# Performance work log

Hardware: AMD Instinct MI355X
Metric: run time of the kernel (lower is better)

Reference implementation:

```python
import jax, jax.numpy as jnp
import numpy as np

THRESHOLD = 0.9
EPS = 1e-12


def setup_inputs() -> dict:
    key = jax.random.key(0)
    ks = jax.random.split(key, 7)
    B, D_in, H1, H2, D_out = 8192, 256, 512, 256, 64
    # torch Linear default init ~ U(-1/sqrt(fan_in), 1/sqrt(fan_in)); randn scaled is fine as a stand-in
    def lin(k, out_f, in_f):
        return jax.random.normal(k, (out_f, in_f), dtype=jnp.float32) / np.sqrt(in_f)
    return {
        "x": jax.random.normal(ks[0], (B, D_in), dtype=jnp.float32),
        "W1": lin(ks[1], H1, D_in),
        "b1": jax.random.normal(ks[2], (H1,), dtype=jnp.float32) * 0.01,
        "W2": lin(ks[3], H2, H1),
        "b2": jax.random.normal(ks[4], (H2,), dtype=jnp.float32) * 0.01,
        "W3": lin(ks[5], D_out, H2),
        "b3": jax.random.normal(ks[6], (D_out,), dtype=jnp.float32) * 0.01,
    }


def reference(x, W1, b1, W2, b2, W3, b3):
    # MLP: Linear -> Tanh -> Linear -> Tanh -> Linear (no tanh on last)
    h1 = jnp.tanh(x @ W1.T + b1)          # [B, 512]
    h2 = jnp.tanh(h1 @ W2.T + b2)         # [B, 256]
    out = h2 @ W3.T + b3                  # [B, 64]

    # Pairwise state fidelity: (normalized dot)^2, thresholded adjacency (diag excluded)
    norms = jnp.linalg.norm(out, axis=-1, keepdims=True)  # [B, 1]
    normed = out / (norms + EPS)
    fid = (normed @ normed.T) ** 2                         # [B, B]
    adj = (fid >= THRESHOLD).astype(out.dtype)
    B = out.shape[0]
    adj = adj * (1.0 - jnp.eye(B, dtype=out.dtype))        # no self-edges (i < j pairs only)

    return adj @ out                                       # [B, 64]
```

## Files before the change

kernel.cpp:

```cpp
#include <hip/hip_runtime.h>
#include <hip/hip_bf16.h>
#include <math.h>

#define B_ROWS 8192
#define D_IN   256
#define H1_DIM 512
#define H2_DIM 256
#define D_OUT  64
#define EPSF   1e-12f
#define THRESH 0.9f
#define BAND_LO 0.89f
#define BAND_HI 0.91f

typedef __attribute__((ext_vector_type(8))) short short8;
typedef __attribute__((ext_vector_type(4))) float f32x4;

__device__ inline float tanh_fast(float xx) {
  const float ax = fabsf(xx);
  const float t = __expf(-2.0f * ax);
  const float r = (1.0f - t) / (1.0f + t);
  return xx < 0.0f ? -r : r;
}

__device__ inline void splitf8(float4 a, float4 b, short8& h, short8& m) {
  float v[8] = {a.x, a.y, a.z, a.w, b.x, b.y, b.z, b.w};
  short h8[8], m8[8];
#pragma unroll
  for (int e = 0; e < 8; ++e) {
    __hip_bfloat16 hb = __float2bfloat16(v[e]);
    float hf = __bfloat162float(hb);
    __hip_bfloat16 mb = __float2bfloat16(v[e] - hf);
    h8[e] = *(short*)&hb;
    m8[e] = *(short*)&mb;
  }
  h = *(short8*)h8;
  m = *(short8*)m8;
}

__global__ __launch_bounds__(512, 2)
void fused_mlp(const float* __restrict__ x,  const float* __restrict__ W1,
               const float* __restrict__ b1, const float* __restrict__ W2,
               const float* __restrict__ b2, const float* __restrict__ W3,
               const float* __restrict__ b3, float* __restrict__ out,
               short* __restrict__ vph, short* __restrict__ vpm,
               float* __restrict__ res) {
  constexpr int WC = 260;
  __shared__ __align__(16) union {
    struct { short h[8192]; short m[8192]; } xp;
    struct { short h[8192]; short m[8192]; } h2p;
  } uAB;
  __shared__ __align__(16) short h1h[16384];
  __shared__ __align__(16) short h1m[16384];
  __shared__ __align__(16) float wbuf[32 * WC];
  __shared__ float nsum[32];
  __shared__ float invn[32];

  const int tid = threadIdx.x;
  const int wave = tid >> 6, lane = tid & 63;
  const int r0 = blockIdx.x * 32;
  const int col16 = lane & 15;
  const int k8 = (lane >> 4) << 3;
  const int rbase = (lane >> 4) * 2 * 2;

  {
    float4* rz = (float4*)(res + (size_t)r0 * D_OUT);
    rz[tid] = make_float4(0.f, 0.f, 0.f, 0.f);
  }

#pragma unroll
  for (int uu = 0; uu < 2; ++uu) {
    const int u = tid + uu * 512;
    const int lu = u & 63, g = u >> 6;
    const int q = g & 7, I = g >> 3;
    const float* p = x + (size_t)(r0 + I * 16 + (lu & 15)) * D_IN + q * 32 + ((lu >> 4) << 3);
    float4 a = *(const float4*)p, b = *(const float4*)(p + 4);
    short8 hh, mm;
    splitf8(a, b, hh, mm);
    const int off = ((I * 8 + q) * 64 + lu) * 8;
    *(short8*)(uAB.xp.h + off) = hh;
    *(short8*)(uAB.xp.m + off) = mm;
  }
  __syncthreads();

  f32x4 acc1[2][4];
#pragma unroll
  for (int it = 0; it < 2; ++it)
#pragma unroll
    for (int jj = 0; jj < 4; ++jj) acc1[it][jj] = (f32x4){0.f, 0.f, 0.f, 0.f};

#pragma unroll 4
  for (int q = 0; q < 8; ++q) {
    short8 Ah[2], Am[2];
#pragma unroll
    for (int it = 0; it < 2; ++it) {
      const int off = ((it * 8 + q) * 64 + lane) * 8;
      Ah[it] = *(const short8*)(uAB.xp.h + off);
      Am[it] = *(const short8*)(uAB.xp.m + off);
    }
    short8 Bh[4], Bm[4];
#pragma unroll
    for (int jj = 0; jj < 4; ++jj) {
      const float* wp = W1 + (size_t)((wave * 4 + jj) * 16 + col16) * D_IN + q * 32 + k8;
      splitf8(*(const float4*)wp, *(const float4*)(wp + 4), Bh[jj], Bm[jj]);
    }
#pragma unroll
    for (int it = 0; it < 2; ++it)
#pragma unroll
      for (int jj = 0; jj < 4; ++jj) {
        acc1[it][jj] = __builtin_amdgcn_mfma_f32_16x16x32_bf16(Ah[it], Bh[jj], acc1[it][jj], 0, 0, 0);
        acc1[it][jj] = __builtin_amdgcn_mfma_f32_16x16x32_bf16(Ah[it], Bm[jj], acc1[it][jj], 0, 0, 0);
        acc1[it][jj] = __builtin_amdgcn_mfma_f32_16x16x32_bf16(Am[it], Bh[jj], acc1[it][jj], 0, 0, 0);
      }
  }

  float bv1[4];
#pragma unroll
  for (int jj = 0; jj < 4; ++jj) bv1[jj] = b1[(wave * 4 + jj) * 16 + col16];

#pragma unroll
  for (int h = 0; h < 2; ++h) {
    if ((wave >> 2) == h) {
#pragma unroll
      for (int it = 0; it < 2; ++it)
#pragma unroll
        for (int jj = 0; jj < 4; ++jj)
#pragma unroll
          for (int r = 0; r < 4; ++r) {
            const int row = it * 16 + rbase + r;
            const int col = ((wave & 3) * 4 + jj) * 16 + col16;
            wbuf[row * WC + col] = tanh_fast(acc1[it][jj][r] + bv1[jj]);
          }
    }
    __syncthreads();
#pragma unroll
    for (int uu = 0; uu < 2; ++uu) {
      const int u = tid + uu * 512;
      const int lu = u & 63, g = u >> 6;
      const int ql = g & 7, it = g >> 3;
      const int row = it * 16 + (lu & 15);
      const int kl = ql * 32 + ((lu >> 4) << 3);
      const float* wp = &wbuf[row * WC + kl];
      short8 hh, mm;
      splitf8(*(const float4*)wp, *(const float4*)(wp + 4), hh, mm);
      const int off = ((it * 16 + h * 8 + ql) * 64 + lu) * 8;
      *(short8*)(h1h + off) = hh;
      *(short8*)(h1m + off) = mm;
    }
    __syncthreads();
  }

  f32x4 acc2[2][2];
#pragma unroll
  for (int it = 0; it < 2; ++it)
#pragma unroll
    for (int jj = 0; jj < 2; ++jj) acc2[it][jj] = (f32x4){0.f, 0.f, 0.f, 0.f};

#pragma unroll 4
  for (int q = 0; q < 16; ++q) {
    short8 Ah[2], Am[2];
#pragma unroll
    for (int it = 0; it < 2; ++it) {
      const int off = ((it * 16 + q) * 64 + lane) * 8;
      Ah[it] = *(const short8*)(h1h + off);
      Am[it] = *(const short8*)(h1m + off);
    }
    short8 Bh[2], Bm[2];
#pragma unroll
    for (int jj = 0; jj < 2; ++jj) {
      const float* wp = W2 + (size_t)((wave * 2 + jj) * 16 + col16) * H1_DIM + q * 32 + k8;
      splitf8(*(const float4*)wp, *(const float4*)(wp + 4), Bh[jj], Bm[jj]);
    }
#pragma unroll
    for (int it = 0; it < 2; ++it)
#pragma unroll
      for (int jj = 0; jj < 2; ++jj) {
        acc2[it][jj] = __builtin_amdgcn_mfma_f32_16x16x32_bf16(Ah[it], Bh[jj], acc2[it][jj], 0, 0, 0);
        acc2[it][jj] = __builtin_amdgcn_mfma_f32_16x16x32_bf16(Ah[it], Bm[jj], acc2[it][jj], 0, 0, 0);
        acc2[it][jj] = __builtin_amdgcn_mfma_f32_16x16x32_bf16(Am[it], Bh[jj], acc2[it][jj], 0, 0, 0);
      }
  }

  {
    float bv2[2];
#pragma unroll
    for (int jj = 0; jj < 2; ++jj) bv2[jj] = b2[(wave * 2 + jj) * 16 + col16];
#pragma unroll
    for (int it = 0; it < 2; ++it)
#pragma unroll
      for (int jj = 0; jj < 2; ++jj)
#pragma unroll
        for (int r = 0; r < 4; ++r) {
          const int row = it * 16 + rbase + r;
          const int col = (wave * 2 + jj) * 16 + col16;
          wbuf[row * WC + col] = tanh_fast(acc2[it][jj][r] + bv2[jj]);
        }
  }
  __syncthreads();
#pragma unroll
  for (int uu = 0; uu < 2; ++uu) {
    const int u = tid + uu * 512;
    const int lu = u & 63, g = u >> 6;
    const int ql = g & 7, it = g >> 3;
    const int row = it * 16 + (lu & 15);
    const int kl = ql * 32 + ((lu >> 4) << 3);
    const float* wp = &wbuf[row * WC + kl];
    short8 hh, mm;
    splitf8(*(const float4*)wp, *(const float4*)(wp + 4), hh, mm);
    const int off = ((it * 8 + ql) * 64 + lu) * 8;
    *(short8*)(uAB.h2p.h + off) = hh;
    *(short8*)(uAB.h2p.m + off) = mm;
  }
  __syncthreads();

  if (wave < 4) {
    f32x4 acc3[2];
#pragma unroll
    for (int it = 0; it < 2; ++it) acc3[it] = (f32x4){0.f, 0.f, 0.f, 0.f};
#pragma unroll
    for (int q = 0; q < 8; ++q) {
      short8 Ah[2], Am[2];
#pragma unroll
      for (int it = 0; it < 2; ++it) {
        const int off = ((it * 8 + q) * 64 + lane) * 8;
        Ah[it] = *(const short8*)(uAB.h2p.h + off);
        Am[it] = *(const short8*)(uAB.h2p.m + off);
      }
      short8 Bh, Bm;
      const float* wp = W3 + (size_t)(wave * 16 + col16) * H2_DIM + q * 32 + k8;
      splitf8(*(const float4*)wp, *(const float4*)(wp + 4), Bh, Bm);
#pragma unroll
      for (int it = 0; it < 2; ++it) {
        acc3[it] = __builtin_amdgcn_mfma_f32_16x16x32_bf16(Ah[it], Bh, acc3[it], 0, 0, 0);
        acc3[it] = __builtin_amdgcn_mfma_f32_16x16x32_bf16(Ah[it], Bm, acc3[it], 0, 0, 0);
        acc3[it] = __builtin_amdgcn_mfma_f32_16x16x32_bf16(Am[it], Bh, acc3[it], 0, 0, 0);
      }
    }
    const float bv3 = b3[wave * 16 + col16];
#pragma unroll
    for (int it = 0; it < 2; ++it)
#pragma unroll
      for (int r = 0; r < 4; ++r)
        wbuf[(it * 16 + rbase + r) * WC + wave * 16 + col16] = acc3[it][r] + bv3;
  }
  __syncthreads();

  if (tid < 256) {
    const int row = tid >> 3, c0 = (tid & 7) * 8;
    const float* wp = &wbuf[row * WC + c0];
    float4 a = *(const float4*)wp, b = *(const float4*)(wp + 4);
    float s = a.x * a.x + a.y * a.y + a.z * a.z + a.w * a.w +
              b.x * b.x + b.y * b.y + b.z * b.z + b.w * b.w;
    s += __shfl_xor(s, 1, 64);
    s += __shfl_xor(s, 2, 64);
    s += __shfl_xor(s, 4, 64);
    if ((tid & 7) == 0) nsum[row] = s;
  }
  __syncthreads();
  if (tid < 32) invn[tid] = 1.0f / (sqrtf(nsum[tid]) + EPSF);
  __syncthreads();

  {
    const int row = tid >> 4, c4 = (tid & 15) * 4;
    *(float4*)(out + (size_t)(r0 + row) * D_OUT + c4) = *(const float4*)&wbuf[row * WC + c4];
  }
  if (tid < 256) {
    const int lu = tid & 63, g = tid >> 6;
    const int ql = g & 1, it = g >> 1;
    const int row = it * 16 + (lu & 15);
    const int kl = ql * 32 + ((lu >> 4) << 3);
    const float sc = invn[row];
    const float* wp = &wbuf[row * WC + kl];
    float4 a = *(const float4*)wp, b = *(const float4*)(wp + 4);
    a.x *= sc; a.y *= sc; a.z *= sc; a.w *= sc;
    b.x *= sc; b.y *= sc; b.z *= sc; b.w *= sc;
    short8 hh, mm;
    splitf8(a, b, hh, mm);
    const size_t off = (((size_t)(blockIdx.x * 2 + it) * 2 + ql) * 64 + lu) * 8;
    *(short8*)(vph + off) = hh;
    *(short8*)(vpm + off) = mm;
  }
}

__global__ __launch_bounds__(256, 2)
void gram_accum(const short* __restrict__ vph, const short* __restrict__ vpm,
                const float* __restrict__ out, float* __restrict__ res) {
  __shared__ __align__(16) short lAh[8 * 1024];
  __shared__ __align__(16) short lAm[8 * 1024];
  const int tid = threadIdx.x;
  const int wave = tid >> 6, lane = tid & 63;

  const int t = blockIdx.x;
  int I = (int)((129.0f - sqrtf(16641.0f - 8.0f * (float)t)) * 0.5f);
  if (I < 0) I = 0;
  while (64 * (I + 1) - ((I + 1) * I) / 2 <= t) ++I;
  while (64 * I - (I * (I - 1)) / 2 > t) --I;
  const int Jc = I + (t - (64 * I - (I * (I - 1)) / 2));
  const int i0 = I * 128;
  const int j0c = Jc * 128;

  {
    const size_t base = (size_t)I * 8192;
#pragma unroll
    for (int u = 0; u < 8; ++u) {
      const int item = wave * 8 + u;
      const short* src;
      short* dst;
      if (item < 16) { src = vph + base + item * 512; dst = lAh + item * 512; }
      else           { src = vpm + base + (item - 16) * 512; dst = lAm + (item - 16) * 512; }
      __builtin_amdgcn_global_load_lds(
          (const __attribute__((address_space(1))) void*)(src + lane * 8),
          (__attribute__((address_space(3))) void*)dst, 16, 0, 0);
    }
  }
  __syncthreads();

  short8 Ah[8][2];
#pragma unroll
  for (int it = 0; it < 8; ++it)
#pragma unroll
    for (int q = 0; q < 2; ++q)
      Ah[it][q] = *(const short8*)(lAh + it * 1024 + q * 512 + lane * 8);

#pragma unroll
  for (int tt = 0; tt < 2; ++tt) {
    const int jt = wave * 2 + tt;
    const int j0 = j0c + jt * 16;
    const short* jb_h = vph + (size_t)(j0 >> 4) * 1024;
    short8 Bh0 = *(const short8*)(jb_h + lane * 8);
    short8 Bh1 = *(const short8*)(jb_h + 512 + lane * 8);

    f32x4 g[8];
#pragma unroll
    for (int it = 0; it < 8; ++it) g[it] = (f32x4){0.f, 0.f, 0.f, 0.f};
#pragma unroll
    for (int it = 0; it < 8; ++it) g[it] = __builtin_amdgcn_mfma_f32_16x16x32_bf16(Ah[it][0], Bh0, g[it], 0, 0, 0);
#pragma unroll
    for (int it = 0; it < 8; ++it) g[it] = __builtin_amdgcn_mfma_f32_16x16x32_bf16(Ah[it][1], Bh1, g[it], 0, 0, 0);

    bool band = false;
#pragma unroll
    for (int it = 0; it < 8; ++it)
#pragma unroll
      for (int r = 0; r < 4; ++r) {
        const float f = g[it][r] * g[it][r];
        band = band || (f > BAND_LO && f < BAND_HI);
      }
    if (__any(band)) {
      const short* jb_m = vpm + (size_t)(j0 >> 4) * 1024;
      short8 Bm0 = *(const short8*)(jb_m + lane * 8);
      short8 Bm1 = *(const short8*)(jb_m + 512 + lane * 8);
#pragma unroll
      for (int it = 0; it < 8; ++it) g[it] = __builtin_amdgcn_mfma_f32_16x16x32_bf16(Ah[it][0], Bm0, g[it], 0, 0, 0);
#pragma unroll
      for (int it = 0; it < 8; ++it) g[it] = __builtin_amdgcn_mfma_f32_16x16x32_bf16(Ah[it][1], Bm1, g[it], 0, 0, 0);
#pragma unroll
      for (int it = 0; it < 8; ++it) {
        short8 Am0 = *(const short8*)(lAm + it * 1024 + lane * 8);
        short8 Am1 = *(const short8*)(lAm + it * 1024 + 512 + lane * 8);
        g[it] = __builtin_amdgcn_mfma_f32_16x16x32_bf16(Am0, Bh0, g[it], 0, 0, 0);
        g[it] = __builtin_amdgcn_mfma_f32_16x16x32_bf16(Am1, Bh1, g[it], 0, 0, 0);
      }
    }

    const int j = j0 + (lane & 15);
#pragma unroll
    for (int it = 0; it < 8; ++it) {
      const float m01 = fmaxf(g[it][0] * g[it][0], g[it][1] * g[it][1]);
      const float m23 = fmaxf(g[it][2] * g[it][2], g[it][3] * g[it][3]);
      if (fmaxf(m01, m23) >= THRESH) {
        const float* __restrict__ oj = out + (size_t)j * D_OUT;
#pragma unroll
        for (int r = 0; r < 4; ++r) {
          if (g[it][r] * g[it][r] >= THRESH) {
            const int i = i0 + it * 16 + (lane >> 4) * 4 + r;
            if (i < j) {
              float* __restrict__ ri = res + (size_t)i * D_OUT;
              float* __restrict__ rj = res + (size_t)j * D_OUT;
              const float* __restrict__ oi = out + (size_t)i * D_OUT;
              for (int k = 0; k < D_OUT; ++k) {
                atomicAdd(&ri[k], oj[k]);
                atomicAdd(&rj[k], oi[k]);
              }
            }
          }
        }
      }
    }
  }
}

#define MB (1024 * 1024)

extern "C" void kernel_launch(void* const* d_in, const int* in_sizes, int n_in,
                              void* d_out, int out_size, void* d_ws, size_t ws_size,
                              hipStream_t stream) {
  const float* x  = (const float*)d_in[0];
  const float* W1 = (const float*)d_in[1];
  const float* b1 = (const float*)d_in[2];
  const float* W2 = (const float*)d_in[3];
  const float* b2 = (const float*)d_in[4];
  const float* W3 = (const float*)d_in[5];
  const float* b3 = (const float*)d_in[6];
  float* res = (float*)d_out;

  char* ws = (char*)d_ws;
  float* out = (float*)(ws);
  short* vph = (short*)(ws + 2 * MB);
  short* vpm = (short*)(ws + 3 * MB);

  fused_mlp<<<256, 512, 0, stream>>>(x, W1, b1, W2, b2, W3, b3, out, vph, vpm, res);
  gram_accum<<<dim3(2080), 256, 0, stream>>>(vph, vpm, out, res);
}
```

Before: 129.1 us.

## Prepack weights, shrink MLP row tile, ballot-based atomic scatter in gram

Adds a weight prepack kernel that splits W1/W2/W3 into bf16 hi/lo fragments once per call, so the fused MLP loads MFMA-ready fragments instead of splitting weights in every block. The MLP now handles 16 rows per block over 512 blocks with a smaller, XOR-swizzled shared buffer to raise occupancy and cut bank conflicts. The gram kernel no longer stages the low-part A tiles in LDS and reads them from global only on band hits. Its per-edge atomic loop becomes a wave ballot where each lane adds one of the 64 columns, giving coalesced atomics. The costs are an extra kernel launch and more workspace.

New measurement: 117.9 us. 1.1x faster.

```diff
diff --git a/kernel.cpp b/kernel.cpp
--- a/kernel.cpp
+++ b/kernel.cpp
@@ -37,245 +37,235 @@
   m = *(short8*)m8;
 }
 
-__global__ __launch_bounds__(512, 2)
-void fused_mlp(const float* __restrict__ x,  const float* __restrict__ W1,
-               const float* __restrict__ b1, const float* __restrict__ W2,
-               const float* __restrict__ b2, const float* __restrict__ W3,
-               const float* __restrict__ b3, float* __restrict__ out,
-               short* __restrict__ vph, short* __restrict__ vpm,
-               float* __restrict__ res) {
-  constexpr int WC = 260;
-  __shared__ __align__(16) union {
-    struct { short h[8192]; short m[8192]; } xp;
-    struct { short h[8192]; short m[8192]; } h2p;
-  } uAB;
-  __shared__ __align__(16) short h1h[16384];
-  __shared__ __align__(16) short h1m[16384];
-  __shared__ __align__(16) float wbuf[32 * WC];
-  __shared__ float nsum[32];
-  __shared__ float invn[32];
+__device__ inline void rd8_swz(const float* buf, int S, int row, int kl,
+                               float4& a, float4& b) {
+  const int xr = (row & 7) << 2;
+  a = *(const float4*)&buf[(row * S + kl) ^ xr];
+  b = *(const float4*)&buf[(row * S + kl + 4) ^ xr];
+}
+
+__device__ inline void pack8(const float* __restrict__ src, short* __restrict__ dh,
+                             short* __restrict__ dm, int t, int C, int lgq) {
+  const int lane = t & 63;
+  const int g = t >> 6;
+  const int q = g & ((1 << lgq) - 1);
+  const int I = g >> lgq;
+  const int row = I * 16 + (lane & 15);
+  const int k0 = q * 32 + ((lane >> 4) << 3);
+  const float* p = src + (size_t)row * C + k0;
+  short8 hh, mm;
+  splitf8(*(const float4*)p, *(const float4*)(p + 4), hh, mm);
+  *(short8*)(dh + (size_t)t * 8) = hh;
+  *(short8*)(dm + (size_t)t * 8) = mm;
+}
+
+__global__ __launch_bounds__(256)
+void wpack(const float* __restrict__ W1, const float* __restrict__ W2,
+           const float* __restrict__ W3,
+           short* w1h, short* w1m, short* w2h, short* w2m,
+           short* w3h, short* w3m) {
+  const int b = blockIdx.x, tid = threadIdx.x;
+  if (b < 64)        pack8(W1, w1h, w1m, b * 256 + tid, 256, 3);
+  else if (b < 128)  pack8(W2, w2h, w2m, (b - 64) * 256 + tid, 512, 4);
+  else               pack8(W3, w3h, w3m, (b - 128) * 256 + tid, 256, 3);
+}
+
+__global__ __launch_bounds__(512, 4)
+void fused_mlp16(const float* __restrict__ x,
+                 const short* __restrict__ w1h, const short* __restrict__ w1m,
+                 const float* __restrict__ b1,
+                 const short* __restrict__ w2h, const short* __restrict__ w2m,
+                 const float* __restrict__ b2,
+                 const short* __restrict__ w3h, const short* __restrict__ w3m,
+                 const float* __restrict__ b3,
+                 float* __restrict__ out, short* __restrict__ vph,
+                 short* __restrict__ vpm, float* __restrict__ res) {
+  __shared__ __align__(16) char smem[49152];
+  short* xph   = (short*)smem;
+  short* xpm   = (short*)(smem + 8192);
+  float* wbuf1 = (float*)smem;
+  float* wbuf3 = (float*)smem;
+  short* h1h   = (short*)(smem + 16384);
+  short* h1m   = (short*)(smem + 32768);
+  float* wbuf2 = (float*)(smem + 16384);
+  short* h2ph  = (short*)(smem + 32768);
+  short* h2pm  = (short*)(smem + 40960);
+  __shared__ float nsum[16];
+  __shared__ float invn[16];
 
   const int tid = threadIdx.x;
   const int wave = tid >> 6, lane = tid & 63;
-  const int r0 = blockIdx.x * 32;
+  const int r0 = blockIdx.x * 16;
   const int col16 = lane & 15;
-  const int k8 = (lane >> 4) << 3;
-  const int rbase = (lane >> 4) * 2 * 2;
-
-  {
+  const int rbase = (lane >> 4) << 2;
+
+  if (tid < 256) {
     float4* rz = (float4*)(res + (size_t)r0 * D_OUT);
     rz[tid] = make_float4(0.f, 0.f, 0.f, 0.f);
   }
 
-#pragma unroll
-  for (int uu = 0; uu < 2; ++uu) {
-    const int u = tid + uu * 512;
-    const int lu = u & 63, g = u >> 6;
-    const int q = g & 7, I = g >> 3;
-    const float* p = x + (size_t)(r0 + I * 16 + (lu & 15)) * D_IN + q * 32 + ((lu >> 4) << 3);
-    float4 a = *(const float4*)p, b = *(const float4*)(p + 4);
+  {
+    const int lu = tid & 63, q = tid >> 6;
+    const float* p = x + (size_t)(r0 + (lu & 15)) * D_IN + q * 32 + ((lu >> 4) << 3);
+    short8 hh, mm;
+    splitf8(*(const float4*)p, *(const float4*)(p + 4), hh, mm);
+    const int off = (q * 64 + lu) * 8;
+    *(short8*)(xph + off) = hh;
+    *(short8*)(xpm + off) = mm;
+  }
+  __syncthreads();
+
+  f32x4 acc1[4];
+#pragma unroll
+  for (int jj = 0; jj < 4; ++jj) acc1[jj] = (f32x4){0.f, 0.f, 0.f, 0.f};
+#pragma unroll 4
+  for (int q = 0; q < 8; ++q) {
+    const int aoff = (q * 64 + lane) * 8;
+    const short8 Ah = *(const short8*)(xph + aoff);
+    const short8 Am = *(const short8*)(xpm + aoff);
+#pragma unroll
+    for (int jj = 0; jj < 4; ++jj) {
+      const int boff = (((wave * 4 + jj) * 8 + q) * 64 + lane) * 8;
+      const short8 Bh = *(const short8*)(w1h + boff);
+      const short8 Bm = *(const short8*)(w1m + boff);
+      acc1[jj] = __builtin_amdgcn_mfma_f32_16x16x32_bf16(Ah, Bh, acc1[jj], 0, 0, 0);
+      acc1[jj] = __builtin_amdgcn_mfma_f32_16x16x32_bf16(Ah, Bm, acc1[jj], 0, 0, 0);
+      acc1[jj] = __builtin_amdgcn_mfma_f32_16x16x32_bf16(Am, Bh, acc1[jj], 0, 0, 0);
+    }
+  }
+  __syncthreads();
+
+  float bv1[4];
+#pragma unroll
+  for (int jj = 0; jj < 4; ++jj) bv1[jj] = b1[(wave * 4 + jj) * 16 + col16];
+#pragma unroll
+  for (int h = 0; h < 2; ++h) {
+    if ((wave >> 2) == h) {
+#pragma unroll
+      for (int jj = 0; jj < 4; ++jj)
+#pragma unroll
+        for (int r = 0; r < 4; ++r) {
+          const int row = rbase + r;
+          const int col = ((wave & 3) * 4 + jj) * 16 + col16;
+          wbuf1[(row * 256 + col) ^ ((row & 7) << 2)] = tanh_fast(acc1[jj][r] + bv1[jj]);
+        }
+    }
+    __syncthreads();
+    {
+      const int lu = tid & 63, ql = tid >> 6;
+      const int row = lu & 15, kl = ql * 32 + ((lu >> 4) << 3);
+      float4 a, b;
+      rd8_swz(wbuf1, 256, row, kl, a, b);
+      short8 hh, mm;
+      splitf8(a, b, hh, mm);
+      const int off = ((h * 8 + ql) * 64 + lu) * 8;
+      *(short8*)(h1h + off) = hh;
+      *(short8*)(h1m + off) = mm;
+    }
+    __syncthreads();
+  }
+
+  f32x4 acc2[2];
+#pragma unroll
+  for (int jj = 0; jj < 2; ++jj) acc2[jj] = (f32x4){0.f, 0.f, 0.f, 0.f};
+#pragma unroll 4
+  for (int q = 0; q < 16; ++q) {
+    const int aoff = (q * 64 + lane) * 8;
+    const short8 Ah = *(const short8*)(h1h + aoff);
+    const short8 Am = *(const short8*)(h1m + aoff);
+#pragma unroll
+    for (int jj = 0; jj < 2; ++jj) {
+      const int boff = (((wave * 2 + jj) * 16 + q) * 64 + lane) * 8;
+      const short8 Bh = *(const short8*)(w2h + boff);
+      const short8 Bm = *(const short8*)(w2m + boff);
+      acc2[jj] = __builtin_amdgcn_mfma_f32_16x16x32_bf16(Ah, Bh, acc2[jj], 0, 0, 0);
+      acc2[jj] = __builtin_amdgcn_mfma_f32_16x16x32_bf16(Ah, Bm, acc2[jj], 0, 0, 0);
+      acc2[jj] = __builtin_amdgcn_mfma_f32_16x16x32_bf16(Am, Bh, acc2[jj], 0, 0, 0);
+    }
+  }
+  __syncthreads();
+
+  {
+    float bv2[2];
+#pragma unroll
+    for (int jj = 0; jj < 2; ++jj) bv2[jj] = b2[(wave * 2 + jj) * 16 + col16];
+#pragma unroll
+    for (int jj = 0; jj < 2; ++jj)
+#pragma unroll
+      for (int r = 0; r < 4; ++r) {
+        const int row = rbase + r;
+        const int col = (wave * 2 + jj) * 16 + col16;
+        wbuf2[(row * 256 + col) ^ ((row & 7) << 2)] = tanh_fast(acc2[jj][r] + bv2[jj]);
+      }
+  }
+  __syncthreads();
+  {
+    const int lu = tid & 63, ql = tid >> 6;
+    const int row = lu & 15, kl = ql * 32 + ((lu >> 4) << 3);
+    float4 a, b;
+    rd8_swz(wbuf2, 256, row, kl, a, b);
     short8 hh, mm;
     splitf8(a, b, hh, mm);
-    const int off = ((I * 8 + q) * 64 + lu) * 8;
-    *(short8*)(uAB.xp.h + off) = hh;
-    *(short8*)(uAB.xp.m + off) = mm;
-  }
-  __syncthreads();
-
-  f32x4 acc1[2][4];
-#pragma unroll
-  for (int it = 0; it < 2; ++it)
-#pragma unroll
-    for (int jj = 0; jj < 4; ++jj) acc1[it][jj] = (f32x4){0.f, 0.f, 0.f, 0.f};
-
+    const int off = (ql * 64 + lu) * 8;
+    *(short8*)(h2ph + off) = hh;
+    *(short8*)(h2pm + off) = mm;
+  }
+  __syncthreads();
+
+  if (wave < 4) {
+    f32x4 acc3 = (f32x4){0.f, 0.f, 0.f, 0.f};
 #pragma unroll 4
-  for (int q = 0; q < 8; ++q) {
-    short8 Ah[2], Am[2];
-#pragma unroll
-    for (int it = 0; it < 2; ++it) {
-      const int off = ((it * 8 + q) * 64 + lane) * 8;
-      Ah[it] = *(const short8*)(uAB.xp.h + off);
-      Am[it] = *(const short8*)(uAB.xp.m + off);
-    }
-    short8 Bh[4], Bm[4];
-#pragma unroll
-    for (int jj = 0; jj < 4; ++jj) {
-      const float* wp = W1 + (size_t)((wave * 4 + jj) * 16 + col16) * D_IN + q * 32 + k8;
-      splitf8(*(const float4*)wp, *(const float4*)(wp + 4), Bh[jj], Bm[jj]);
-    }
-#pragma unroll
-    for (int it = 0; it < 2; ++it)
-#pragma unroll
-      for (int jj = 0; jj < 4; ++jj) {
-        acc1[it][jj] = __builtin_amdgcn_mfma_f32_16x16x32_bf16(Ah[it], Bh[jj], acc1[it][jj], 0, 0, 0);
-        acc1[it][jj] = __builtin_amdgcn_mfma_f32_16x16x32_bf16(Ah[it], Bm[jj], acc1[it][jj], 0, 0, 0);
-        acc1[it][jj] = __builtin_amdgcn_mfma_f32_16x16x32_bf16(Am[it], Bh[jj], acc1[it][jj], 0, 0, 0);
-      }
-  }
-
-  float bv1[4];
-#pragma unroll
-  for (int jj = 0; jj < 4; ++jj) bv1[jj] = b1[(wave * 4 + jj) * 16 + col16];
-
-#pragma unroll
-  for (int h = 0; h < 2; ++h) {
-    if ((wave >> 2) == h) {
-#pragma unroll
-      for (int it = 0; it < 2; ++it)
-#pragma unroll
-        for (int jj = 0; jj < 4; ++jj)
-#pragma unroll
-          for (int r = 0; r < 4; ++r) {
-            const int row = it * 16 + rbase + r;
-            const int col = ((wave & 3) * 4 + jj) * 16 + col16;
-            wbuf[row * WC + col] = tanh_fast(acc1[it][jj][r] + bv1[jj]);
-          }
-    }
-    __syncthreads();
-#pragma unroll
-    for (int uu = 0; uu < 2; ++uu) {
-      const int u = tid + uu * 512;
-      const int lu = u & 63, g = u >> 6;
-      const int ql = g & 7, it = g >> 3;
-      const int row = it * 16 + (lu & 15);
-      const int kl = ql * 32 + ((lu >> 4) << 3);
-      const float* wp = &wbuf[row * WC + kl];
-      short8 hh, mm;
-      splitf8(*(const float4*)wp, *(const float4*)(wp + 4), hh, mm);
-      const int off = ((it * 16 + h * 8 + ql) * 64 + lu) * 8;
-      *(short8*)(h1h + off) = hh;
-      *(short8*)(h1m + off) = mm;
-    }
-    __syncthreads();
-  }
-
-  f32x4 acc2[2][2];
-#pragma unroll
-  for (int it = 0; it < 2; ++it)
-#pragma unroll
-    for (int jj = 0; jj < 2; ++jj) acc2[it][jj] = (f32x4){0.f, 0.f, 0.f, 0.f};
-
-#pragma unroll 4
-  for (int q = 0; q < 16; ++q) {
-    short8 Ah[2], Am[2];
-#pragma unroll
-    for (int it = 0; it < 2; ++it) {
-      const int off = ((it * 16 + q) * 64 + lane) * 8;
-      Ah[it] = *(const short8*)(h1h + off);
-      Am[it] = *(const short8*)(h1m + off);
-    }
-    short8 Bh[2], Bm[2];
-#pragma unroll
-    for (int jj = 0; jj < 2; ++jj) {
-      const float* wp = W2 + (size_t)((wave * 2 + jj) * 16 + col16) * H1_DIM + q * 32 + k8;
-      splitf8(*(const float4*)wp, *(const float4*)(wp + 4), Bh[jj], Bm[jj]);
-    }
-#pragma unroll
-    for (int it = 0; it < 2; ++it)
-#pragma unroll
-      for (int jj = 0; jj < 2; ++jj) {
-        acc2[it][jj] = __builtin_amdgcn_mfma_f32_16x16x32_bf16(Ah[it], Bh[jj], acc2[it][jj], 0, 0, 0);
-        acc2[it][jj] = __builtin_amdgcn_mfma_f32_16x16x32_bf16(Ah[it], Bm[jj], acc2[it][jj], 0, 0, 0);
-        acc2[it][jj] = __builtin_amdgcn_mfma_f32_16x16x32_bf16(Am[it], Bh[jj], acc2[it][jj], 0, 0, 0);
-      }
-  }
-
-  {
-    float bv2[2];
-#pragma unroll
-    for (int jj = 0; jj < 2; ++jj) bv2[jj] = b2[(wave * 2 + jj) * 16 + col16];
-#pragma unroll
-    for (int it = 0; it < 2; ++it)
-#pragma unroll
-      for (int jj = 0; jj < 2; ++jj)
-#pragma unroll
-        for (int r = 0; r < 4; ++r) {
-          const int row = it * 16 + rbase + r;
-          const int col = (wave * 2 + jj) * 16 + col16;
-          wbuf[row * WC + col] = tanh_fast(acc2[it][jj][r] + bv2[jj]);
-        }
-  }
-  __syncthreads();
-#pragma unroll
-  for (int uu = 0; uu < 2; ++uu) {
-    const int u = tid + uu * 512;
-    const int lu = u & 63, g = u >> 6;
-    const int ql = g & 7, it = g >> 3;
-    const int row = it * 16 + (lu & 15);
-    const int kl = ql * 32 + ((lu >> 4) << 3);
-    const float* wp = &wbuf[row * WC + kl];
-    short8 hh, mm;
-    splitf8(*(const float4*)wp, *(const float4*)(wp + 4), hh, mm);
-    const int off = ((it * 8 + ql) * 64 + lu) * 8;
-    *(short8*)(uAB.h2p.h + off) = hh;
-    *(short8*)(uAB.h2p.m + off) = mm;
-  }
-  __syncthreads();
-
-  if (wave < 4) {
-    f32x4 acc3[2];
-#pragma unroll
-    for (int it = 0; it < 2; ++it) acc3[it] = (f32x4){0.f, 0.f, 0.f, 0.f};
-#pragma unroll
     for (int q = 0; q < 8; ++q) {
-      short8 Ah[2], Am[2];
-#pragma unroll
-      for (int it = 0; it < 2; ++it) {
-        const int off = ((it * 8 + q) * 64 + lane) * 8;
-        Ah[it] = *(const short8*)(uAB.h2p.h + off);
-        Am[it] = *(const short8*)(uAB.h2p.m + off);
-      }
-      short8 Bh, Bm;
-      const float* wp = W3 + (size_t)(wave * 16 + col16) * H2_DIM + q * 32 + k8;
-      splitf8(*(const float4*)wp, *(const float4*)(wp + 4), Bh, Bm);
-#pragma unroll
-      for (int it = 0; it < 2; ++it) {
-        acc3[it] = __builtin_amdgcn_mfma_f32_16x16x32_bf16(Ah[it], Bh, acc3[it], 0, 0, 0);
-        acc3[it] = __builtin_amdgcn_mfma_f32_16x16x32_bf16(Ah[it], Bm, acc3[it], 0, 0, 0);
-        acc3[it] = __builtin_amdgcn_mfma_f32_16x16x32_bf16(Am[it], Bh, acc3[it], 0, 0, 0);
-      }
+      const int aoff = (q * 64 + lane) * 8;
+      const short8 Ah = *(const short8*)(h2ph + aoff);
+      const short8 Am = *(const short8*)(h2pm + aoff);
+      const int boff = ((wave * 8 + q) * 64 + lane) * 8;
+      const short8 Bh = *(const short8*)(w3h + boff);
+      const short8 Bm = *(const short8*)(w3m + boff);
+      acc3 = __builtin_amdgcn_mfma_f32_16x16x32_bf16(Ah, Bh, acc3, 0, 0, 0);
+      acc3 = __builtin_amdgcn_mfma_f32_16x16x32_bf16(Ah, Bm, acc3, 0, 0, 0);
+      acc3 = __builtin_amdgcn_mfma_f32_16x16x32_bf16(Am, Bh, acc3, 0, 0, 0);
     }
     const float bv3 = b3[wave * 16 + col16];
 #pragma unroll
-    for (int it = 0; it < 2; ++it)
-#pragma unroll
-      for (int r = 0; r < 4; ++r)
-        wbuf[(it * 16 + rbase + r) * WC + wave * 16 + col16] = acc3[it][r] + bv3;
+    for (int r = 0; r < 4; ++r) {
+      const int row = rbase + r;
+      const int col = wave * 16 + col16;
+      wbuf3[(row * 64 + col) ^ ((row & 7) << 2)] = acc3[r] + bv3;
+    }
   }
   __syncthreads();
 
   if (tid < 256) {
-    const int row = tid >> 3, c0 = (tid & 7) * 8;
-    const float* wp = &wbuf[row * WC + c0];
-    float4 a = *(const float4*)wp, b = *(const float4*)(wp + 4);
-    float s = a.x * a.x + a.y * a.y + a.z * a.z + a.w * a.w +
-              b.x * b.x + b.y * b.y + b.z * b.z + b.w * b.w;
+    const int row = tid >> 4, c4 = (tid & 15) * 4;
+    const float4 a = *(const float4*)&wbuf3[(row * 64 + c4) ^ ((row & 7) << 2)];
+    float s = a.x * a.x + a.y * a.y + a.z * a.z + a.w * a.w;
     s += __shfl_xor(s, 1, 64);
     s += __shfl_xor(s, 2, 64);
     s += __shfl_xor(s, 4, 64);
-    if ((tid & 7) == 0) nsum[row] = s;
-  }
-  __syncthreads();
-  if (tid < 32) invn[tid] = 1.0f / (sqrtf(nsum[tid]) + EPSF);
-  __syncthreads();
-
-  {
+    s += __shfl_xor(s, 8, 64);
+    if ((tid & 15) == 0) nsum[row] = s;
+  }
+  __syncthreads();
+  if (tid < 16) invn[tid] = 1.0f / (sqrtf(nsum[tid]) + EPSF);
+  __syncthreads();
+
+  if (tid < 256) {
     const int row = tid >> 4, c4 = (tid & 15) * 4;
-    *(float4*)(out + (size_t)(r0 + row) * D_OUT + c4) = *(const float4*)&wbuf[row * WC + c4];
-  }
-  if (tid < 256) {
-    const int lu = tid & 63, g = tid >> 6;
-    const int ql = g & 1, it = g >> 1;
-    const int row = it * 16 + (lu & 15);
-    const int kl = ql * 32 + ((lu >> 4) << 3);
+    *(float4*)(out + (size_t)(r0 + row) * D_OUT + c4) =
+        *(const float4*)&wbuf3[(row * 64 + c4) ^ ((row & 7) << 2)];
+  }
+  if (tid < 128) {
+    const int lu = tid & 63, ql = tid >> 6;
+    const int row = lu & 15, kl = ql * 32 + ((lu >> 4) << 3);
     const float sc = invn[row];
-    const float* wp = &wbuf[row * WC + kl];
-    float4 a = *(const float4*)wp, b = *(const float4*)(wp + 4);
+    float4 a, b;
+    rd8_swz(wbuf3, 64, row, kl, a, b);
     a.x *= sc; a.y *= sc; a.z *= sc; a.w *= sc;
     b.x *= sc; b.y *= sc; b.z *= sc; b.w *= sc;
     short8 hh, mm;
     splitf8(a, b, hh, mm);
-    const size_t off = (((size_t)(blockIdx.x * 2 + it) * 2 + ql) * 64 + lu) * 8;
+    const size_t off = (((size_t)blockIdx.x * 2 + ql) * 64 + lu) * 8;
     *(short8*)(vph + off) = hh;
     *(short8*)(vpm + off) = mm;
   }
@@ -285,7 +275,6 @@
 void gram_accum(const short* __restrict__ vph, const short* __restrict__ vpm,
                 const float* __restrict__ out, float* __restrict__ res) {
   __shared__ __align__(16) short lAh[8 * 1024];
-  __shared__ __align__(16) short lAm[8 * 1024];
   const int tid = threadIdx.x;
   const int wave = tid >> 6, lane = tid & 63;
 
@@ -301,15 +290,11 @@
   {
     const size_t base = (size_t)I * 8192;
 #pragma unroll
-    for (int u = 0; u < 8; ++u) {
-      const int item = wave * 8 + u;
-      const short* src;
-      short* dst;
-      if (item < 16) { src = vph + base + item * 512; dst = lAh + item * 512; }
-      else           { src = vpm + base + (item - 16) * 512; dst = lAm + (item - 16) * 512; }
+    for (int u = 0; u < 4; ++u) {
+      const int item = wave * 4 + u;
       __builtin_amdgcn_global_load_lds(
-          (const __attribute__((address_space(1))) void*)(src + lane * 8),
-          (__attribute__((address_space(3))) void*)dst, 16, 0, 0);
+          (const __attribute__((address_space(1))) void*)(vph + base + item * 512 + lane * 8),
+          (__attribute__((address_space(3))) void*)(lAh + item * 512), 16, 0, 0);
     }
   }
   __syncthreads();
@@ -355,41 +340,36 @@
       for (int it = 0; it < 8; ++it) g[it] = __builtin_amdgcn_mfma_f32_16x16x32_bf16(Ah[it][1], Bm1, g[it], 0, 0, 0);
 #pragma unroll
       for (int it = 0; it < 8; ++it) {
-        short8 Am0 = *(const short8*)(lAm + it * 1024 + lane * 8);
-        short8 Am1 = *(const short8*)(lAm + it * 1024 + 512 + lane * 8);
+        const size_t abase = (size_t)((i0 >> 4) + it) * 1024;
+        short8 Am0 = *(const short8*)(vpm + abase + lane * 8);
+        short8 Am1 = *(const short8*)(vpm + abase + 512 + lane * 8);
         g[it] = __builtin_amdgcn_mfma_f32_16x16x32_bf16(Am0, Bh0, g[it], 0, 0, 0);
         g[it] = __builtin_amdgcn_mfma_f32_16x16x32_bf16(Am1, Bh1, g[it], 0, 0, 0);
       }
     }
 
-    const int j = j0 + (lane & 15);
-#pragma unroll
-    for (int it = 0; it < 8; ++it) {
-      const float m01 = fmaxf(g[it][0] * g[it][0], g[it][1] * g[it][1]);
-      const float m23 = fmaxf(g[it][2] * g[it][2], g[it][3] * g[it][3]);
-      if (fmaxf(m01, m23) >= THRESH) {
-        const float* __restrict__ oj = out + (size_t)j * D_OUT;
-#pragma unroll
-        for (int r = 0; r < 4; ++r) {
-          if (g[it][r] * g[it][r] >= THRESH) {
-            const int i = i0 + it * 16 + (lane >> 4) * 4 + r;
-            if (i < j) {
-              float* __restrict__ ri = res + (size_t)i * D_OUT;
-              float* __restrict__ rj = res + (size_t)j * D_OUT;
-              const float* __restrict__ oi = out + (size_t)i * D_OUT;
-              for (int k = 0; k < D_OUT; ++k) {
-                atomicAdd(&ri[k], oj[k]);
-                atomicAdd(&rj[k], oi[k]);
-              }
-            }
-          }
+    const int jl = j0 + (lane & 15);
+#pragma unroll
+    for (int it = 0; it < 8; ++it)
+#pragma unroll
+      for (int r = 0; r < 4; ++r) {
+        const int il = i0 + it * 16 + (lane >> 4) * 4 + r;
+        unsigned long long m =
+            __ballot((g[it][r] * g[it][r] >= THRESH) && (il < jl));
+        while (m) {
+          const int s = __builtin_ctzll(m);
+          m &= m - 1;
+          const int js = j0 + (s & 15);
+          const int is = i0 + it * 16 + ((s >> 4) << 2) + r;
+          atomicAdd(res + (size_t)is * D_OUT + lane, out[(size_t)js * D_OUT + lane]);
+          atomicAdd(res + (size_t)js * D_OUT + lane, out[(size_t)is * D_OUT + lane]);
         }
       }
-    }
   }
 }
 
 #define MB (1024 * 1024)
+#define KB 1024
 
 extern "C" void kernel_launch(void* const* d_in, const int* in_sizes, int n_in,
                               void* d_out, int out_size, void* d_ws, size_t ws_size,
@@ -407,7 +387,15 @@
   float* out = (float*)(ws);
   short* vph = (short*)(ws + 2 * MB);
   short* vpm = (short*)(ws + 3 * MB);
-
-  fused_mlp<<<256, 512, 0, stream>>>(x, W1, b1, W2, b2, W3, b3, out, vph, vpm, res);
+  short* w1h = (short*)(ws + 4 * MB);
+  short* w1m = (short*)(ws + 4 * MB + 256 * KB);
+  short* w2h = (short*)(ws + 4 * MB + 512 * KB);
+  short* w2m = (short*)(ws + 4 * MB + 768 * KB);
+  short* w3h = (short*)(ws + 5 * MB);
+  short* w3m = (short*)(ws + 5 * MB + 32 * KB);
+
+  wpack<<<136, 256, 0, stream>>>(W1, W2, W3, w1h, w1m, w2h, w2m, w3h, w3m);
+  fused_mlp16<<<512, 512, 0, stream>>>(x, w1h, w1m, b1, w2h, w2m, b2,
+                                       w3h, w3m, b3, out, vph, vpm, res);
   gram_accum<<<dim3(2080), 256, 0, stream>>>(vph, vpm, out, res);
 }
```
